# Kernel optimization log

Hardware: AMD Instinct MI355X
Metric: run time of the kernel (lower is better)

The kernel has to match this reference:

```python
import jax, jax.numpy as jnp
import numpy as np

FS = 16000.0
SOUND_SPEED = 343.0
MAX_ORDER = 10
FILTER_LEN = 81            # fractional-delay sinc filter taps (torchaudio default)
PAD = FILTER_LEN // 2      # 40
RIR_LEN = 8000             # static RIR length; bounds max delay for 10 m rooms, order 10

# ---- static image-source lattice: all (i,j,k) with |i|+|j|+|k| <= MAX_ORDER ----
_ind = np.arange(-MAX_ORDER, MAX_ORDER + 1)
_g = np.stack(np.meshgrid(_ind, _ind, _ind, indexing="ij"), -1).reshape(-1, 3)
_g = _g[np.abs(_g).sum(-1) <= MAX_ORDER]                      # (n_img=1561, 3)
XYZ = jnp.asarray(_g, dtype=jnp.float32)                      # (n_img, 3)
EXP_LO = jnp.asarray(np.abs(np.floor(_g / 2.0)), jnp.float32)        # reflections off x=0/y=0/z=0 walls
EXP_HI = jnp.asarray(np.abs(np.floor((_g + 1) / 2.0)), jnp.float32)  # reflections off far walls
ODD = jnp.asarray(_g % 2 == 1)                                # (n_img, 3) bool


def _hann(x, T):
    # truncated Hann window used by the fractional-delay filter
    return jnp.where(jnp.abs(x) <= T / 2, 0.5 * (1.0 + jnp.cos(2.0 * jnp.pi * x / T)), 0.0)


def _rir_one(room, mic, src, absorption):
    # room, mic, src: (3,) metres; absorption: (6,) per-wall absorption coeff
    # image-source positions: mirror source across walls per parity of lattice index
    img = jnp.where(ODD, room * (XYZ + 1.0) - src, room * XYZ + src)   # (n_img, 3)
    tr = jnp.sqrt(1.0 - absorption)                                     # wall reflection coeffs (6,)
    att = jnp.prod((tr[::2] ** EXP_LO) * (tr[1::2] ** EXP_HI), axis=-1)  # (n_img,)
    dist = jnp.linalg.norm(img - mic, axis=-1)                           # (n_img,)
    amp = att / dist                                                     # 1/r spreading
    delay = dist * FS / SOUND_SPEED                                      # delay in samples (float)
    delay_i = jnp.ceil(delay)                                            # integer anchor
    n = jnp.arange(-PAD, PAD + 1, dtype=jnp.float32)                     # (81,)
    x = n[None, :] + delay_i[:, None] - delay[:, None]                   # (n_img, 81)
    irs = amp[:, None] * jnp.sinc(x) * _hann(x, 2 * PAD)                 # windowed-sinc frac delay
    # scatter-add each 81-tap filter at offset delay_i - PAD into the RIR buffer
    idx = delay_i.astype(jnp.int32)[:, None] - PAD + jnp.arange(FILTER_LEN, dtype=jnp.int32)
    valid = (idx >= 0) & (idx < RIR_LEN)
    rir = jnp.zeros((RIR_LEN,), irs.dtype).at[jnp.clip(idx, 0, RIR_LEN - 1)].add(
        jnp.where(valid, irs, 0.0))
    return rir


def setup_inputs() -> dict:
    key = jax.random.key(0)
    k1, k2, k3, k4 = jax.random.split(key, 4)
    B = 256
    room = 3.0 + 7.0 * jax.random.uniform(k1, (B, 3), jnp.float32)       # room dims in [3,10] m
    mic_f = 0.05 + 0.40 * jax.random.uniform(k2, (B, 3), jnp.float32)    # mic frac in [0.05,0.45]
    src_f = 0.55 + 0.40 * jax.random.uniform(k3, (B, 3), jnp.float32)    # src frac in [0.55,0.95]
    absorp = 0.1 + 0.4 * jax.random.uniform(k4, (B, 1), jnp.float32)     # absorption in [0.1,0.5]
    inp = jnp.concatenate([room, mic_f, src_f, absorp], axis=1)          # (B, 10)
    return {"input": inp}


def reference(input):
    room = input[:, 0:3]
    mic = input[:, 3:6] * room
    src = input[:, 6:9] * room
    absorption = jnp.repeat(input[:, 9:10], 6, axis=1)                   # uniform over 6 walls
    rir = jax.vmap(_rir_one)(room, mic, src, absorption)                 # (B, RIR_LEN)
    dist = jnp.linalg.norm(mic - src, axis=1)
    toa = 40.0 + FS * dist / SOUND_SPEED                                 # (B,)
    return rir, toa
```

## Files before the change

### kernel.cpp

```cpp
#include <hip/hip_runtime.h>
#include <math.h>

#define NB 256
#define NIMG 1561
#define RIRLEN 8000
#define PADI 40
#define NTHREADS 1024
#define NWAVES (NTHREADS / 64)
#define NBKT 505
#define NSTARTP 512
#define NPAIR 63

struct ImgTab { unsigned int v[NIMG]; };

constexpr ImgTab build_tab() {
    ImgTab t{};
    int n = 0;
    for (int x = -10; x <= 10; ++x)
        for (int y = -10; y <= 10; ++y)
            for (int z = -10; z <= 10; ++z) {
                int ax = x < 0 ? -x : x;
                int ay = y < 0 ? -y : y;
                int az = z < 0 ? -z : z;
                int l1 = ax + ay + az;
                if (l1 <= 10) {
                    t.v[n++] = (unsigned)(x + 10) | ((unsigned)(y + 10) << 5) |
                               ((unsigned)(z + 10) << 10) | ((unsigned)l1 << 15);
                }
            }
    return t;
}

constexpr int tab_count() {
    int n = 0;
    for (int x = -10; x <= 10; ++x)
        for (int y = -10; y <= 10; ++y)
            for (int z = -10; z <= 10; ++z) {
                int ax = x < 0 ? -x : x;
                int ay = y < 0 ? -y : y;
                int az = z < 0 ? -z : z;
                if (ax + ay + az <= 10) ++n;
            }
    return n;
}
static_assert(tab_count() == NIMG, "image count mismatch");

__constant__ ImgTab c_tab = build_tab();

__global__ __launch_bounds__(NTHREADS) void
rir_kernel(const float* __restrict__ in, float* __restrict__ out) {
    __shared__ float4 s_rec[NIMG + 1];
    __shared__ float  s_trpow[11];
    __shared__ int    s_hist[NBKT];
    __shared__ int    s_scan[512];
    __shared__ int    s_start[NSTARTP];
    __shared__ int    s_cursor[NBKT];
    __shared__ int    s_qnext;
    __shared__ int    s_nspike;
    __shared__ int    s_spike_idx[64];
    __shared__ float  s_spike_amp[64];

    const int b   = blockIdx.x;
    const int tid = threadIdx.x;
    const float* p = in + b * 10;

    if (tid < NBKT) s_hist[tid] = 0;
    if (tid == 0) {
        float tr = sqrtf(1.0f - p[9]);
        float pw = 1.0f;
        for (int k = 0; k <= 10; ++k) { s_trpow[k] = pw; pw *= tr; }
        s_nspike = 0;
        s_qnext  = NWAVES;
        s_rec[NIMG] = make_float4(0.0f, 0.0f, 0.0f, -1.0e6f);
    }
    __syncthreads();

    const float rx = p[0], ry = p[1], rz = p[2];
    const float mx = p[3] * rx, my = p[4] * ry, mz = p[5] * rz;
    const float sx = p[6] * rx, sy = p[7] * ry, sz = p[8] * rz;
    const float K = 16000.0f / 343.0f;
    const float INV_PI = 0.31830988618379067154f;

    float4 rec[2];
    int ibkt[2]  = {0, 0};
    bool ivalid[2] = {false, false};

    for (int u = 0; u < 2; ++u) {
        int i = tid + u * NTHREADS;
        if (i < NIMG) {
            unsigned v = c_tab.v[i];
            int gx = (int)(v & 31u) - 10;
            int gy = (int)((v >> 5) & 31u) - 10;
            int gz = (int)((v >> 10) & 31u) - 10;
            int l1 = (int)(v >> 15);

            float ix = (gx & 1) ? rx * (float)(gx + 1) - sx : rx * (float)gx + sx;
            float iy = (gy & 1) ? ry * (float)(gy + 1) - sy : ry * (float)gy + sy;
            float iz = (gz & 1) ? rz * (float)(gz + 1) - sz : rz * (float)gz + sz;

            float dx = ix - mx, dy = iy - my, dz = iz - mz;
            float dist = sqrtf(dx * dx + dy * dy + dz * dz);

            float amp  = s_trpow[l1] / dist;
            float d    = dist * K;
            float dlc  = ceilf(d);
            float frac = dlc - d;
            int   idlc = (int)dlc;
            int   base = idlc - PADI;

            if (base < RIRLEN) {
                if (frac == 0.0f) {
                    if (idlc < RIRLEN) {
                        int sp = atomicAdd(&s_nspike, 1);
                        if (sp < 64) { s_spike_idx[sp] = idlc; s_spike_amp[sp] = amp; }
                    }
                } else {
                    float spf = (frac < 1.0e-3f) ? frac : (sinpif(frac) * INV_PI);
                    float S   = amp * spf;
                    if (idlc & 1) S = -S;
                    float hS  = 0.5f * S;
                    float cd  = cospif(d * 0.025f);
                    float sd  = sinpif(d * 0.025f);
                    rec[u] = make_float4(hS, hS * cd, hS * sd, d);
                    ibkt[u]   = (base + 80) >> 4;
                    ivalid[u] = true;
                    atomicAdd(&s_hist[ibkt[u]], 1);
                }
            }
        }
    }
    __syncthreads();

    if (tid < 512) s_scan[tid] = (tid < NBKT) ? s_hist[tid] : 0;
    __syncthreads();
    for (int d = 1; d < 512; d <<= 1) {
        int y = 0;
        if (tid < 512 && tid >= d) y = s_scan[tid - d];
        __syncthreads();
        if (tid < 512) s_scan[tid] += y;
        __syncthreads();
    }
    if (tid < NBKT) {
        s_start[tid + 1] = s_scan[tid];
        s_cursor[tid]    = (tid == 0) ? 0 : s_scan[tid - 1];
        if (tid == 0) s_start[0] = 0;
    }
    if (tid >= NBKT + 1 && tid < NSTARTP) s_start[tid] = s_scan[NBKT - 1];
    __syncthreads();

    for (int u = 0; u < 2; ++u) {
        if (ivalid[u]) {
            int pos = atomicAdd(&s_cursor[ibkt[u]], 1);
            s_rec[pos] = rec[u];
        }
    }
    __syncthreads();

    const int wave = tid >> 6;
    const int lane = tid & 63;
    const int h    = lane >> 5;
    const int l5   = lane & 31;
    const float sgn  = (l5 & 1) ? -1.0f : 1.0f;
    const float vinf = __builtin_inff();
    float* __restrict__ ob = out + (size_t)b * RIRLEN;

    int q = wave;
    while (q < NPAIR) {
        const int n0 = (q << 7) + (h << 6) + l5;
        const int n1 = n0 + 32;
        const float fn0 = (float)n0;
        const float cn0 = cospif(fn0 * 0.025f), sn0 = sinpif(fn0 * 0.025f);
        const float cn1 = -sn0, sn1 = cn0;
        const float c32 = cospif(0.8f), s32 = sinpif(0.8f);
        const float cnn1 = cn0 * c32 - sn0 * s32;
        const float snn1 = sn0 * c32 + cn0 * s32;
        (void)cn1; (void)sn1;

        const int loA = s_start[8 * q];
        const int hiA = s_start[8 * q + 9];
        const int loB = s_start[8 * q + 4];
        const int hiB = s_start[8 * q + 13];
        const int lenA = hiA - loA, lenB = hiB - loB;
        const int lmin = (lenA < lenB) ? lenA : lenB;
        const int lmax = (lenA > lenB) ? lenA : lenB;
        const int lo   = h ? loB : loA;
        const int hi   = h ? hiB : hiA;

        float acc0 = 0.0f, acc1 = 0.0f;
#pragma clang loop unroll_count(8)
        for (int it = 0; it < lmin; ++it) {
            float4 r = s_rec[lo + it];
            float x0 = fn0 - r.w;
            float x1 = x0 + 32.0f;
            float xm0 = (fabsf(x0) < 40.0f) ? x0 : vinf;
            float xm1 = (fabsf(x1) < 40.0f) ? x1 : vinf;
            float t0 = fmaf(r.y, cn0, r.x);  t0 = fmaf(r.z, sn0, t0);
            float t1 = fmaf(r.y, cnn1, r.x); t1 = fmaf(r.z, snn1, t1);
            acc0 = fmaf(t0, __builtin_amdgcn_rcpf(xm0), acc0);
            acc1 = fmaf(t1, __builtin_amdgcn_rcpf(xm1), acc1);
        }
        for (int it = lmin; it < lmax; ++it) {
            int k = lo + it;
            float4 r = s_rec[(k < hi) ? k : NIMG];
            float x0 = fn0 - r.w;
            float x1 = x0 + 32.0f;
            float xm0 = (fabsf(x0) < 40.0f) ? x0 : vinf;
            float xm1 = (fabsf(x1) < 40.0f) ? x1 : vinf;
            float t0 = fmaf(r.y, cn0, r.x);  t0 = fmaf(r.z, sn0, t0);
            float t1 = fmaf(r.y, cnn1, r.x); t1 = fmaf(r.z, snn1, t1);
            acc0 = fmaf(t0, __builtin_amdgcn_rcpf(xm0), acc0);
            acc1 = fmaf(t1, __builtin_amdgcn_rcpf(xm1), acc1);
        }
        if (n0 < RIRLEN) ob[n0] = acc0 * sgn;
        if (n1 < RIRLEN) ob[n1] = acc1 * sgn;

        int nq;
        if (lane == 0) nq = atomicAdd(&s_qnext, 1);
        q = __shfl(nq, 0);
    }

    __syncthreads();
    int nsp = s_nspike; nsp = (nsp < 64) ? nsp : 64;
    if (tid < nsp) atomicAdd(&ob[s_spike_idx[tid]], s_spike_amp[tid]);

    if (tid == 0) {
        float dx = mx - sx, dy = my - sy, dz = mz - sz;
        out[(size_t)NB * RIRLEN + b] = 40.0f + sqrtf(dx * dx + dy * dy + dz * dz) * K;
    }
}

extern "C" void kernel_launch(void* const* d_in, const int* in_sizes, int n_in,
                              void* d_out, int out_size, void* d_ws, size_t ws_size,
                              hipStream_t stream) {
    const float* in = (const float*)d_in[0];
    float* out = (float*)d_out;
    rir_kernel<<<dim3(NB), dim3(NTHREADS), 0, stream>>>(in, out);
}
```

Measured before the change: 80.67 us.

## Split each batch item across two blocks and use wave-shuffle bucket scan

Launches two blocks per batch item, and each block gathers only half of the output chunk pairs. Both blocks redundantly recompute all image sources and the bucket sort. The 512-entry shared-memory Hillis-Steele scan, which needed many barriers, is replaced by a single-wave scan that gives each lane 8 buckets and combines them with shuffles. The rotation constants are hoisted as literals. This trades duplicated setup work for more blocks per GPU, which should help fill the MI355X's compute units better than 256 blocks do.

```diff
diff --git a/kernel.cpp b/kernel.cpp
--- a/kernel.cpp
+++ b/kernel.cpp
@@ -51,8 +51,7 @@
 rir_kernel(const float* __restrict__ in, float* __restrict__ out) {
     __shared__ float4 s_rec[NIMG + 1];
     __shared__ float  s_trpow[11];
-    __shared__ int    s_hist[NBKT];
-    __shared__ int    s_scan[512];
+    __shared__ int    s_hist[NSTARTP];
     __shared__ int    s_start[NSTARTP];
     __shared__ int    s_cursor[NBKT];
     __shared__ int    s_qnext;
@@ -60,17 +59,21 @@
     __shared__ int    s_spike_idx[64];
     __shared__ float  s_spike_amp[64];
 
-    const int b   = blockIdx.x;
-    const int tid = threadIdx.x;
+    const int b    = blockIdx.x >> 1;
+    const int half = blockIdx.x & 1;
+    const int tid  = threadIdx.x;
     const float* p = in + b * 10;
 
-    if (tid < NBKT) s_hist[tid] = 0;
+    const int qlo = half ? 32 : 0;
+    const int qhi = half ? NPAIR : 32;
+
+    if (tid < NSTARTP) s_hist[tid] = 0;
     if (tid == 0) {
         float tr = sqrtf(1.0f - p[9]);
         float pw = 1.0f;
         for (int k = 0; k <= 10; ++k) { s_trpow[k] = pw; pw *= tr; }
         s_nspike = 0;
-        s_qnext  = NWAVES;
+        s_qnext  = qlo + NWAVES;
         s_rec[NIMG] = make_float4(0.0f, 0.0f, 0.0f, -1.0e6f);
     }
     __syncthreads();
@@ -131,21 +134,31 @@
     }
     __syncthreads();
 
-    if (tid < 512) s_scan[tid] = (tid < NBKT) ? s_hist[tid] : 0;
-    __syncthreads();
-    for (int d = 1; d < 512; d <<= 1) {
-        int y = 0;
-        if (tid < 512 && tid >= d) y = s_scan[tid - d];
-        __syncthreads();
-        if (tid < 512) s_scan[tid] += y;
-        __syncthreads();
-    }
-    if (tid < NBKT) {
-        s_start[tid + 1] = s_scan[tid];
-        s_cursor[tid]    = (tid == 0) ? 0 : s_scan[tid - 1];
-        if (tid == 0) s_start[0] = 0;
-    }
-    if (tid >= NBKT + 1 && tid < NSTARTP) s_start[tid] = s_scan[NBKT - 1];
+    if (tid < 64) {
+        int base_i = tid * 8;
+        int v[8], pre[8];
+        int run = 0;
+#pragma unroll
+        for (int j = 0; j < 8; ++j) {
+            v[j] = s_hist[base_i + j];
+            pre[j] = run;
+            run += v[j];
+        }
+        int t = run;
+#pragma unroll
+        for (int d2 = 1; d2 < 64; d2 <<= 1) {
+            int y = __shfl_up(t, d2);
+            if (tid >= d2) t += y;
+        }
+        int excl = t - run;
+#pragma unroll
+        for (int j = 0; j < 8; ++j) {
+            int idx = base_i + j;
+            int sv  = excl + pre[j];
+            s_start[idx] = sv;
+            if (idx < NBKT) s_cursor[idx] = sv;
+        }
+    }
     __syncthreads();
 
     for (int u = 0; u < 2; ++u) {
@@ -162,19 +175,18 @@
     const int l5   = lane & 31;
     const float sgn  = (l5 & 1) ? -1.0f : 1.0f;
     const float vinf = __builtin_inff();
+    const float c32  = -0.80901699437494742410f;
+    const float s32  =  0.58778525229247312917f;
     float* __restrict__ ob = out + (size_t)b * RIRLEN;
 
-    int q = wave;
-    while (q < NPAIR) {
+    int q = qlo + wave;
+    while (q < qhi) {
         const int n0 = (q << 7) + (h << 6) + l5;
         const int n1 = n0 + 32;
         const float fn0 = (float)n0;
         const float cn0 = cospif(fn0 * 0.025f), sn0 = sinpif(fn0 * 0.025f);
-        const float cn1 = -sn0, sn1 = cn0;
-        const float c32 = cospif(0.8f), s32 = sinpif(0.8f);
         const float cnn1 = cn0 * c32 - sn0 * s32;
         const float snn1 = sn0 * c32 + cn0 * s32;
-        (void)cn1; (void)sn1;
 
         const int loA = s_start[8 * q];
         const int hiA = s_start[8 * q + 9];
@@ -221,9 +233,14 @@
 
     __syncthreads();
     int nsp = s_nspike; nsp = (nsp < 64) ? nsp : 64;
-    if (tid < nsp) atomicAdd(&ob[s_spike_idx[tid]], s_spike_amp[tid]);
-
-    if (tid == 0) {
+    if (tid < nsp) {
+        int idx = s_spike_idx[tid];
+        int rlo = half ? 4096 : 0;
+        int rhi = half ? RIRLEN : 4096;
+        if (idx >= rlo && idx < rhi) atomicAdd(&ob[idx], s_spike_amp[tid]);
+    }
+
+    if (tid == 0 && half == 0) {
         float dx = mx - sx, dy = my - sy, dz = mz - sz;
         out[(size_t)NB * RIRLEN + b] = 40.0f + sqrtf(dx * dx + dy * dy + dz * dz) * K;
     }
@@ -234,5 +251,5 @@
                               hipStream_t stream) {
     const float* in = (const float*)d_in[0];
     float* out = (float*)d_out;
-    rir_kernel<<<dim3(NB), dim3(NTHREADS), 0, stream>>>(in, out);
-}
+    rir_kernel<<<dim3(NB * 2), dim3(NTHREADS), 0, stream>>>(in, out);
+}
```

New measurement: 89.29 us. +10.7%, slower.
